# Kernel optimization log

Measured on AMD Instinct MI355X. Metric: run time of the kernel, lower is better.

## Reference

```python
import jax, jax.numpy as jnp
import numpy as np

K = 8        # args.num_k
SEARCH = 4   # search_range -> 9x9 window
LEVELS = 5


def setup_inputs() -> dict:
    key = jax.random.key(0)
    k1, k2, k3 = jax.random.split(key, 3)
    B, C, H, W = 2, 256, 64, 96
    fmap1 = jax.random.normal(k1, (B, C, H, W), jnp.float32)
    fmap2 = jax.random.normal(k2, (B, C, H, W), jnp.float32)
    flow = jax.random.normal(k3, (B, 2, H, W), jnp.float32)
    return {"fmap1": fmap1, "fmap2": fmap2, "flow": flow}


def _sparse_corr_pyramid(fmap1, fmap2, flow):
    B, C, H, W = fmap1.shape
    N = H * W
    WIN = 2 * SEARCH + 1  # 9
    f1 = fmap1.reshape(B, C, N)
    f2 = fmap2.reshape(B, C, N)

    # ---- kNN via full inner-product + top_k (indices are no-grad constants) ----
    corr_full = jnp.einsum('bcn,bcm->bnm', jax.lax.stop_gradient(f1), jax.lax.stop_gradient(f2))
    _, idx = jax.lax.top_k(corr_full, K)  # [B,N,K]

    # ---- differentiable gather of fmap2 at kNN indices + correlation ----
    idx_b = jnp.broadcast_to(idx.reshape(B, 1, N * K), (B, C, N * K))
    f2g = jnp.take_along_axis(f2, idx_b, axis=2).reshape(B, C, N, K)
    corr_sp = jnp.einsum('bcn,bcnk->bkn', f1, f2g) / jnp.sqrt(jnp.float32(C))  # [B,K,N]

    # ---- displacement coords (y-first grid), shifted by flow (no-grad) ----
    ys, xs = jnp.meshgrid(jnp.arange(H), jnp.arange(W), indexing='ij')
    grid = jnp.stack([ys.reshape(-1), xs.reshape(-1)], 0).astype(jnp.float32)  # [2,N]
    coords1 = jnp.transpose(grid[:, idx], (1, 0, 3, 2))  # [B,2,K,N] target (y,x)
    disp = coords1 - grid[None, :, None, :]              # coords1 - coords0
    flow_yx = flow.reshape(B, 2, N)[:, ::-1]             # flow[:, [1,0]]
    disp = jax.lax.stop_gradient(disp - flow_yx[:, :, None, :])  # [B,2,K,N]

    off = jnp.array([[0., 0.], [0., 1.], [1., 0.], [1., 1.]], jnp.float32)  # 4 bilinear corners
    b_idx = jnp.arange(B).reshape(B, 1, 1, 1)
    pix = jnp.arange(N).reshape(1, 1, 1, N)  # pixel flat index = y*W + x (row-major)

    levels = []
    for i in range(LEVELS):
        c = disp * (0.5 ** i)                                  # [B,2,K,N]
        corner = jnp.floor(c)[:, :, None] + off.T[None, :, :, None, None]  # [B,2,4,K,N]
        # bilinear weights (computed under no_grad in torch)
        w = jax.lax.stop_gradient(jnp.prod(1.0 - jnp.abs(c[:, :, None] - corner), axis=1))  # [B,4,K,N]
        mask = (jnp.abs(corner[:, 0]) <= SEARCH) & (jnp.abs(corner[:, 1]) <= SEARCH)
        vals = jnp.where(mask, w * corr_sp[:, None], 0.0)      # [B,4,K,N]
        dy = jnp.clip(corner[:, 0].astype(jnp.int32) + SEARCH, 0, WIN - 1)
        dx = jnp.clip(corner[:, 1].astype(jnp.int32) + SEARCH, 0, WIN - 1)
        flat = ((b_idx * N + pix) * WIN + dy) * WIN + dx       # [B,4,K,N]
        dense = jnp.zeros((B * N * WIN * WIN,), vals.dtype)
        dense = dense.at[flat.reshape(-1)].add(vals.reshape(-1))  # duplicate-index add == coalesce
        levels.append(dense.reshape(B, H, W, WIN * WIN))
    corr = jnp.concatenate(levels, axis=3)                     # [B,H,W,405]
    return jnp.transpose(corr, (0, 3, 1, 2))                   # [B,405,H,W]


def reference(fmap1, fmap2, flow):
    return _sparse_corr_pyramid(fmap1, fmap2, flow)
```

## Files before the change

kernel.cpp:

```cpp
#include <hip/hip_runtime.h>
#include <math.h>

#define Bn 2
#define Cc 256
#define Hh 64
#define Ww 96
#define Nn (Hh*Ww)
#define NLEV 5
#define SCH 4
#define CPC (Nn/SCH)
#define ROWT 48
#define NITER (CPC/128)
#define HOIST 3
#define TKEEP 6
#define KNEG __uint_as_float(0xFF7FFFFFu)

typedef __bf16 bf16x8 __attribute__((ext_vector_type(8)));
typedef float f32x4v __attribute__((ext_vector_type(4)));

#define KEY_INS(k, VA, LEN) do {                                          \
  float _c = (k);                                                         \
  _Pragma("unroll")                                                       \
  for (int _s = 0; _s < (LEN); ++_s) {                                    \
    float _h = fmaxf(VA[_s], _c);                                         \
    _c = fminf(VA[_s], _c);                                               \
    VA[_s] = _h;                                                          \
  }                                                                       \
} while (0)

#define TOPK_INS(v, ix, VA, IA, LEN) do {                                 \
  if ((v) > VA[(LEN)-1]) {                                                \
    VA[(LEN)-1] = (v); IA[(LEN)-1] = (ix);                                \
    _Pragma("unroll")                                                     \
    for (int _s = (LEN)-1; _s > 0; --_s) {                                \
      if (VA[_s] > VA[_s-1]) {                                            \
        float _t = VA[_s]; VA[_s] = VA[_s-1]; VA[_s-1] = _t;              \
        int   _u = IA[_s]; IA[_s] = IA[_s-1]; IA[_s-1] = _u;              \
      }                                                                   \
    }                                                                     \
  }                                                                       \
} while (0)

__device__ __forceinline__ void gld16(const void* g, void* l) {
  __builtin_amdgcn_global_load_lds(
      (const __attribute__((address_space(1))) void*)g,
      (__attribute__((address_space(3))) void*)l, 16, 0, 0);
}

__device__ inline unsigned short f2bf(float f) {
  __bf16 h = (__bf16)f;
  return __builtin_bit_cast(unsigned short, h);
}

__global__ __launch_bounds__(256) void transpose_convert(
    const float* __restrict__ f1, const float* __restrict__ f2,
    __bf16* __restrict__ t1b, __bf16* __restrict__ t2b,
    float* __restrict__ t1f, float* __restrict__ t2f)
{
  __shared__ float tile[64][65];
  const int tid = threadIdx.x;
  const int bid = blockIdx.x;
  const int map = bid / 768;
  const int rem = bid % 768;
  const int b   = rem / 384;
  const int r2  = rem % 384;
  const int c0  = (r2 / 96) * 64;
  const int n0  = (r2 % 96) * 64;

  const float* src = (map ? f2 : f1) + (size_t)b*Cc*Nn;
  __bf16* dstb = (map ? t2b : t1b) + (size_t)b*Nn*Cc;
  float*  dstf = (map ? t2f : t1f) + (size_t)b*Nn*Cc;

  const int nl = tid & 63;
  const int cb = tid >> 6;
  #pragma unroll
  for (int i = 0; i < 16; ++i) {
    const int c = cb + i*4;
    tile[nl][c] = src[(size_t)(c0 + c)*Nn + n0 + nl];
  }
  __syncthreads();
  #pragma unroll
  for (int j = 0; j < 4; ++j) {
    const int idx = j*256 + tid;
    const int n = idx >> 4, c4 = idx & 15;
    float v0 = tile[n][c4*4+0], v1 = tile[n][c4*4+1];
    float v2 = tile[n][c4*4+2], v3 = tile[n][c4*4+3];
    const size_t obase = (size_t)(n0 + n)*Cc + c0 + c4*4;
    float4 vf = make_float4(v0, v1, v2, v3);
    *(float4*)(dstf + obase) = vf;
    ushort4 ub = make_ushort4(f2bf(v0), f2bf(v1), f2bf(v2), f2bf(v3));
    *(ushort4*)(dstb + obase) = ub;
  }
}

__global__ __launch_bounds__(256, 4) void mfma_prefilter(
    const __bf16* __restrict__ f1t, const __bf16* __restrict__ f2t,
    unsigned* __restrict__ pv)
{
  __shared__ __align__(16) char smem[40960];
  unsigned* mk = (unsigned*)smem;

  const int tid  = threadIdx.x;
  const int lane = tid & 63;
  const int wv   = tid >> 6;
  const int bid  = blockIdx.x;
  const int b    = bid / (128*SCH);
  const int r2   = bid % (128*SCH);
  const int row0 = (r2 >> 2) * ROWT;
  const int sc   = r2 & 3;
  const int col0 = sc * CPC;
  const size_t bN = (size_t)b * Nn;

  #pragma unroll
  for (int i = 0; i < 6; ++i) {
    const int seg = wv*6 + i;
    const int row = seg*2 + (lane >> 5);
    const int gs  = lane & 31;
    const __bf16* gp = f1t + ((bN + row0 + row) << 8) + ((gs ^ (row & 7)) << 3);
    gld16(gp, smem + seg*1024);
  }

  size_t offB[2];
  #pragma unroll
  for (int i = 0; i < 2; ++i) {
    const int cl = wv*32 + i*16 + (lane >> 2);
    const int g2 = (lane & 3) ^ ((cl >> 1) & 3);
    offB[i] = ((bN + col0 + cl) << 8) + (g2 << 3);
  }
  #define STAGE_B(q, elemoff) do {                                        \
    _Pragma("unroll")                                                     \
    for (int _i = 0; _i < 2; ++_i)                                        \
      gld16(f2t + offB[_i] + (elemoff),                                   \
            smem + 24576 + (q)*8192 + wv*2048 + _i*1024);                 \
  } while (0)

  STAGE_B(0, 0);
  asm volatile("s_waitcnt vmcnt(2)" ::: "memory");
  __builtin_amdgcn_sched_barrier(0);
  __syncthreads();

  bf16x8 bfrH[3][HOIST];
  #pragma unroll
  for (int kc = 0; kc < HOIST; ++kc)
    #pragma unroll
    for (int cg = 0; cg < 3; ++cg) {
      const int rw = cg*16 + (lane & 15);
      const int gas = (kc*4 + (lane >> 4)) ^ (rw & 7);
      bfrH[cg][kc] = *(const bf16x8*)((const char*)smem + rw*512 + gas*16);
    }

  float va[3][TKEEP];
  #pragma unroll
  for (int cg = 0; cg < 3; ++cg)
    #pragma unroll
    for (int j = 0; j < TKEEP; ++j) va[cg][j] = KNEG;

  for (int iter = 0; iter < NITER; ++iter) {
    f32x4v acc[2][3];
    #pragma unroll
    for (int rg = 0; rg < 2; ++rg)
      #pragma unroll
      for (int cg = 0; cg < 3; ++cg)
        acc[rg][cg] = (f32x4v){0.f, 0.f, 0.f, 0.f};

    #pragma unroll
    for (int kc = 0; kc < 8; ++kc) {
      if (kc < 7) {
        STAGE_B((kc+1)&1, (size_t)iter*32768 + (kc+1)*32);
        asm volatile("s_waitcnt vmcnt(2)" ::: "memory");
      } else if (iter < NITER-1) {
        STAGE_B(0, (size_t)(iter+1)*32768);
        asm volatile("s_waitcnt vmcnt(2)" ::: "memory");
      } else {
        asm volatile("s_waitcnt vmcnt(0)" ::: "memory");
      }
      __builtin_amdgcn_sched_barrier(0);

      bf16x8 af[2], bfr[3];
      const int q = kc & 1;
      #pragma unroll
      for (int rg = 0; rg < 2; ++rg) {
        const int cl = wv*32 + rg*16 + (lane & 15);
        const int gsw = (lane >> 4) ^ ((cl >> 1) & 3);
        af[rg] = *(const bf16x8*)(smem + 24576 + q*8192 + cl*64 + gsw*16);
      }
      #pragma unroll
      for (int cg = 0; cg < 3; ++cg) {
        if (kc < HOIST) {
          bfr[cg] = bfrH[cg][kc];
        } else {
          const int rw = cg*16 + (lane & 15);
          const int gas = (kc*4 + (lane >> 4)) ^ (rw & 7);
          bfr[cg] = *(const bf16x8*)((const char*)smem + rw*512 + gas*16);
        }
      }
      __builtin_amdgcn_s_setprio(1);
      #pragma unroll
      for (int rg = 0; rg < 2; ++rg)
        #pragma unroll
        for (int cg = 0; cg < 3; ++cg)
          acc[rg][cg] = __builtin_amdgcn_mfma_f32_16x16x32_bf16(
              af[rg], bfr[cg], acc[rg][cg], 0, 0, 0);
      __builtin_amdgcn_s_setprio(0);
    }

    const int colB = col0 + iter*128 + wv*32 + ((lane >> 4) << 2);
    #pragma unroll
    for (int cg = 0; cg < 3; ++cg)
      #pragma unroll
      for (int rg = 0; rg < 2; ++rg)
        #pragma unroll
        for (int j = 0; j < 4; ++j) {
          const unsigned u =
              (__float_as_uint(acc[rg][cg][j]) & 0xFFFFE000u) |
              (unsigned)(colB + rg*16 + j);
          KEY_INS(__uint_as_float(u), va[cg], TKEEP);
        }
  }

  __syncthreads();
  const int slot = wv*4 + (lane >> 4);
  #pragma unroll
  for (int cg = 0; cg < 3; ++cg) {
    const int row = cg*16 + (lane & 15);
    #pragma unroll
    for (int j = 0; j < TKEEP; ++j)
      mk[row*97 + slot*TKEEP + j] = __float_as_uint(va[cg][j]);
  }
  __syncthreads();
  if (tid < ROWT) {
    float tv[8];
    #pragma unroll
    for (int j = 0; j < 8; ++j) tv[j] = KNEG;
    for (int e = 0; e < 16*TKEEP; ++e)
      KEY_INS(__uint_as_float(mk[tid*97 + e]), tv, 8);
    const size_t base = (bN + row0 + tid)*32 + sc*8;
    #pragma unroll
    for (int j = 0; j < 8; ++j) pv[base + j] = __float_as_uint(tv[j]);
  }
}

__global__ __launch_bounds__(256) void rescore_select(
    const unsigned* __restrict__ pv,
    const float* __restrict__ t1f, const float* __restrict__ t2f,
    float* __restrict__ fv, int* __restrict__ fi)
{
  __shared__ float f1s[8][256];
  __shared__ int   cidx[8][16];
  __shared__ float cex[8][16];

  const int tid = threadIdx.x;
  const int bid = blockIdx.x;
  const int b   = bid / 768;
  const int n0  = (bid % 768) * 8;
  const size_t bn0 = (size_t)b*Nn + n0;

  #pragma unroll
  for (int k = 0; k < 2; ++k) {
    const int idx = k*256 + tid;
    const int r = idx >> 6, p = idx & 63;
    *(float4*)(&f1s[r][p*4]) = *(const float4*)(t1f + (bn0 + r)*256 + p*4);
  }

  if (tid < 8) {
    float va[16];
    #pragma unroll
    for (int j = 0; j < 16; ++j) va[j] = KNEG;
    const size_t base = (bn0 + tid)*32;
    for (int e = 0; e < 32; ++e)
      KEY_INS(__uint_as_float(pv[base + e]), va, 16);
    #pragma unroll
    for (int j = 0; j < 16; ++j)
      cidx[tid][j] = (int)(__float_as_uint(va[j]) & 0x1FFFu);
  }
  __syncthreads();

  {
    const int lane = tid & 63;
    const int cg = lane >> 3, li = lane & 7;
    #pragma unroll
    for (int nn = 0; nn < 2; ++nn) {
      const int nl = (tid >> 6)*2 + nn;
      #pragma unroll
      for (int p = 0; p < 2; ++p) {
        const int cand = p*8 + cg;
        const int m = cidx[nl][cand];
        const float4* p2 = (const float4*)(t2f + ((size_t)b*Nn + m)*256);
        float sum = 0.f;
        #pragma unroll
        for (int j = 0; j < 8; ++j) {
          const int fi4 = j*8 + li;
          float4 a = *(const float4*)(&f1s[nl][fi4*4]);
          float4 c = p2[fi4];
          sum += a.x*c.x + a.y*c.y + a.z*c.z + a.w*c.w;
        }
        sum += __shfl_xor(sum, 1);
        sum += __shfl_xor(sum, 2);
        sum += __shfl_xor(sum, 4);
        if (li == 0) cex[nl][cand] = sum;
      }
    }
  }
  __syncthreads();

  if (tid < 8) {
    float va[8]; int ia[8];
    #pragma unroll
    for (int j = 0; j < 8; ++j) { va[j] = -INFINITY; ia[j] = 0; }
    #pragma unroll
    for (int e = 0; e < 16; ++e)
      TOPK_INS(cex[tid][e], cidx[tid][e], va, ia, 8);
    const size_t base = (bn0 + tid)*8;
    #pragma unroll
    for (int j = 0; j < 8; ++j) { fv[base+j] = va[j]; fi[base+j] = ia[j]; }
  }
}

__global__ __launch_bounds__(128) void pyramid_kernel(
    const float* __restrict__ fv, const int* __restrict__ fi,
    const float* __restrict__ flow, float* __restrict__ out)
{
  __shared__ float accs[128*81];
  const int tid = threadIdx.x;
  const int g   = blockIdx.x*128 + tid;
  const int lvl = blockIdx.y;
  const int b   = g / Nn;
  const int n   = g % Nn;

  float tvv[8]; int ti[8];
  #pragma unroll
  for (int k = 0; k < 8; ++k) { tvv[k] = fv[(size_t)g*8 + k]; ti[k] = fi[(size_t)g*8 + k]; }

  const int y = n / Ww, x = n % Ww;
  const float fly = flow[((size_t)b*2 + 1)*Nn + n];
  const float flx = flow[((size_t)b*2 + 0)*Nn + n];
  const float scale = 1.0f / (float)(1 << lvl);

  float* lacc = &accs[tid*81];
  #pragma unroll
  for (int c2 = 0; c2 < 81; ++c2) lacc[c2] = 0.f;

  #pragma unroll
  for (int k = 0; k < 8; ++k) {
    const int m  = ti[k];
    const int ym = m / Ww, xm = m % Ww;
    const float val = tvv[k] * 0.0625f;
    const float cy = ((float)(ym - y) - fly) * scale;
    const float cx = ((float)(xm - x) - flx) * scale;
    const float fy0 = floorf(cy), fx0 = floorf(cx);
    const float ry = cy - fy0, rx = cx - fx0;
    const int iy = (int)fy0, ix = (int)fx0;
    if (iy   >= -4 && iy   <= 4 && ix   >= -4 && ix   <= 4)
      lacc[(iy+4)*9 + (ix+4)]     += (1.f-ry)*(1.f-rx)*val;
    if (iy   >= -4 && iy   <= 4 && ix+1 >= -4 && ix+1 <= 4)
      lacc[(iy+4)*9 + (ix+1+4)]   += (1.f-ry)*rx*val;
    if (iy+1 >= -4 && iy+1 <= 4 && ix   >= -4 && ix   <= 4)
      lacc[(iy+1+4)*9 + (ix+4)]   += ry*(1.f-rx)*val;
    if (iy+1 >= -4 && iy+1 <= 4 && ix+1 >= -4 && ix+1 <= 4)
      lacc[(iy+1+4)*9 + (ix+1+4)] += ry*rx*val;
  }

  const size_t obase = ((size_t)b*(NLEV*81) + lvl*81) * Nn + n;
  #pragma unroll
  for (int c2 = 0; c2 < 81; ++c2)
    out[obase + (size_t)c2*Nn] = lacc[c2];
}

extern "C" void kernel_launch(void* const* d_in, const int* in_sizes, int n_in,
                              void* d_out, int out_size, void* d_ws, size_t ws_size,
                              hipStream_t stream) {
  const float* fmap1 = (const float*)d_in[0];
  const float* fmap2 = (const float*)d_in[1];
  const float* flow  = (const float*)d_in[2];
  float* out = (float*)d_out;

  char* w = (char*)d_ws;
  const size_t szBf  = (size_t)Bn*Nn*Cc*sizeof(unsigned short);
  const size_t szF   = (size_t)Bn*Nn*Cc*sizeof(float);
  const size_t szPv  = (size_t)Bn*Nn*32*sizeof(unsigned);
  const size_t szFv  = (size_t)Bn*Nn*8*sizeof(float);

  __bf16*   t1b = (__bf16*)(w);
  __bf16*   t2b = (__bf16*)(w + szBf);
  float*    t1f = (float*)(w + 2*szBf);
  float*    t2f = (float*)(w + 2*szBf + szF);
  unsigned* pv  = (unsigned*)(w + 2*szBf + 2*szF);
  float*    fv  = (float*)(w + 2*szBf + 2*szF + szPv);
  int*      fi  = (int*)  (w + 2*szBf + 2*szF + szPv + szFv);

  transpose_convert<<<dim3(1536), dim3(256), 0, stream>>>(fmap1, fmap2, t1b, t2b, t1f, t2f);
  mfma_prefilter  <<<dim3(Bn*128*SCH), dim3(256), 0, stream>>>(t1b, t2b, pv);
  rescore_select  <<<dim3(1536), dim3(256), 0, stream>>>(pv, t1f, t2f, fv, fi);
  pyramid_kernel  <<<dim3(96, NLEV), dim3(128), 0, stream>>>(fv, fi, flow, out);
}
```

Before: 177.3 us.

## Hold full fmap1 tile in registers, shrink LDS, skip top-k inserts via wave vote

The fmap1 row tile is no longer staged through LDS. All 8 k-chunks of A fragments are loaded straight from global memory into registers before the main loop, which removes the initial barrier and the per-iteration LDS reads. LDS use drops to just the double-buffered fmap2 stage plus the merge scratch. In the top-k update, each group of four candidate keys is first compared against the current threshold, and the insertion network is skipped when no lane in the wave needs it. The extra register pressure forces launch bounds down from 4 to 3 waves per SIMD, which may reduce latency hiding.

```diff
diff --git a/kernel.cpp b/kernel.cpp
--- a/kernel.cpp
+++ b/kernel.cpp
@@ -11,7 +11,6 @@
 #define CPC (Nn/SCH)
 #define ROWT 48
 #define NITER (CPC/128)
-#define HOIST 3
 #define TKEEP 6
 #define KNEG __uint_as_float(0xFF7FFFFFu)
 
@@ -93,11 +92,11 @@
   }
 }
 
-__global__ __launch_bounds__(256, 4) void mfma_prefilter(
+__global__ __launch_bounds__(256, 3) void mfma_prefilter(
     const __bf16* __restrict__ f1t, const __bf16* __restrict__ f2t,
     unsigned* __restrict__ pv)
 {
-  __shared__ __align__(16) char smem[40960];
+  __shared__ __align__(16) char smem[18688];
   unsigned* mk = (unsigned*)smem;
 
   const int tid  = threadIdx.x;
@@ -111,14 +110,15 @@
   const int col0 = sc * CPC;
   const size_t bN = (size_t)b * Nn;
 
-  #pragma unroll
-  for (int i = 0; i < 6; ++i) {
-    const int seg = wv*6 + i;
-    const int row = seg*2 + (lane >> 5);
-    const int gs  = lane & 31;
-    const __bf16* gp = f1t + ((bN + row0 + row) << 8) + ((gs ^ (row & 7)) << 3);
-    gld16(gp, smem + seg*1024);
-  }
+  bf16x8 bfrH[3][8];
+  #pragma unroll
+  for (int kc = 0; kc < 8; ++kc)
+    #pragma unroll
+    for (int cg = 0; cg < 3; ++cg) {
+      const int rw = cg*16 + (lane & 15);
+      bfrH[cg][kc] = *(const bf16x8*)(
+          f1t + ((bN + row0 + rw) << 8) + kc*32 + ((lane >> 4) << 3));
+    }
 
   size_t offB[2];
   #pragma unroll
@@ -131,23 +131,12 @@
     _Pragma("unroll")                                                     \
     for (int _i = 0; _i < 2; ++_i)                                        \
       gld16(f2t + offB[_i] + (elemoff),                                   \
-            smem + 24576 + (q)*8192 + wv*2048 + _i*1024);                 \
+            smem + (q)*8192 + wv*2048 + _i*1024);                         \
   } while (0)
 
   STAGE_B(0, 0);
   asm volatile("s_waitcnt vmcnt(2)" ::: "memory");
   __builtin_amdgcn_sched_barrier(0);
-  __syncthreads();
-
-  bf16x8 bfrH[3][HOIST];
-  #pragma unroll
-  for (int kc = 0; kc < HOIST; ++kc)
-    #pragma unroll
-    for (int cg = 0; cg < 3; ++cg) {
-      const int rw = cg*16 + (lane & 15);
-      const int gas = (kc*4 + (lane >> 4)) ^ (rw & 7);
-      bfrH[cg][kc] = *(const bf16x8*)((const char*)smem + rw*512 + gas*16);
-    }
 
   float va[3][TKEEP];
   #pragma unroll
@@ -176,23 +165,13 @@
       }
       __builtin_amdgcn_sched_barrier(0);
 
-      bf16x8 af[2], bfr[3];
+      bf16x8 af[2];
       const int q = kc & 1;
       #pragma unroll
       for (int rg = 0; rg < 2; ++rg) {
         const int cl = wv*32 + rg*16 + (lane & 15);
         const int gsw = (lane >> 4) ^ ((cl >> 1) & 3);
-        af[rg] = *(const bf16x8*)(smem + 24576 + q*8192 + cl*64 + gsw*16);
-      }
-      #pragma unroll
-      for (int cg = 0; cg < 3; ++cg) {
-        if (kc < HOIST) {
-          bfr[cg] = bfrH[cg][kc];
-        } else {
-          const int rw = cg*16 + (lane & 15);
-          const int gas = (kc*4 + (lane >> 4)) ^ (rw & 7);
-          bfr[cg] = *(const bf16x8*)((const char*)smem + rw*512 + gas*16);
-        }
+        af[rg] = *(const bf16x8*)(smem + q*8192 + cl*64 + gsw*16);
       }
       __builtin_amdgcn_s_setprio(1);
       #pragma unroll
@@ -200,7 +179,7 @@
         #pragma unroll
         for (int cg = 0; cg < 3; ++cg)
           acc[rg][cg] = __builtin_amdgcn_mfma_f32_16x16x32_bf16(
-              af[rg], bfr[cg], acc[rg][cg], 0, 0, 0);
+              af[rg], bfrH[cg][kc], acc[rg][cg], 0, 0, 0);
       __builtin_amdgcn_s_setprio(0);
     }
 
@@ -208,14 +187,22 @@
     #pragma unroll
     for (int cg = 0; cg < 3; ++cg)
       #pragma unroll
-      for (int rg = 0; rg < 2; ++rg)
+      for (int rg = 0; rg < 2; ++rg) {
+        float k4[4];
         #pragma unroll
         for (int j = 0; j < 4; ++j) {
           const unsigned u =
               (__float_as_uint(acc[rg][cg][j]) & 0xFFFFE000u) |
               (unsigned)(colB + rg*16 + j);
-          KEY_INS(__uint_as_float(u), va[cg], TKEEP);
+          k4[j] = __uint_as_float(u);
         }
+        const float gmax = fmaxf(fmaxf(k4[0], k4[1]), fmaxf(k4[2], k4[3]));
+        if (__any(gmax > va[cg][TKEEP-1])) {
+          #pragma unroll
+          for (int j = 0; j < 4; ++j)
+            KEY_INS(k4[j], va[cg], TKEEP);
+        }
+      }
   }
 
   __syncthreads();
```

Result: slower. 186.7 us (+5.3%).
